# Kernel tuning notes

Hardware: AMD Instinct MI355X
Metric: run time of the kernel (lower is better)

The kernel has to match this reference:

```python
import jax, jax.numpy as jnp
import numpy as np

N, M, H, EMB, F = 2000, 32, 64, 32, 32   # nodes, neighbors, hidden, emb_dim, node_feat_dim
T, B, HOR = 12, 4, 12                     # seq_len, batch, horizon
K = 2                                     # tcn kernel
L_SAGE = 2
DILS = (1, 2)                             # dilations for the 2 TCN blocks


def _causal_conv(x, w, b, d):
    # x: (BN, C, T), w: (C_out, C_in, K) -- causal via left padding (K-1)*d
    y = jax.lax.conv_general_dilated(
        x, w, window_strides=(1,), padding=[((K - 1) * d, 0)],
        rhs_dilation=(d,), dimension_numbers=('NCH', 'OIH', 'NCH'))
    return y + b[None, :, None]


def setup_inputs() -> dict:
    key = jax.random.key(0)
    ks = jax.random.split(key, 32)
    s = 0.05
    def g(i, shape):
        return jax.random.normal(ks[i], shape, dtype=jnp.float32) * s
    return dict(
        inputs=jax.random.normal(ks[0], (T, B, N), dtype=jnp.float32),
        node_feas=jax.random.normal(ks[1], (N, F), dtype=jnp.float32),
        node_index=jax.random.randint(ks[2], (N, M), 0, N),
        # NodeEmbeddingMLP (fc3/fc4/fc5)
        w_fc3=g(3, (F, H)), b_fc3=jnp.zeros((H,), jnp.float32),
        w_fc4=g(4, (H, H)), b_fc4=jnp.zeros((H,), jnp.float32),
        w_fc5=g(5, (H, EMB)), b_fc5=jnp.zeros((EMB,), jnp.float32),
        # node_hidden_proj
        w_nhp=g(6, (EMB, H)), b_nhp=jnp.zeros((H,), jnp.float32),
        # attention (no bias)
        w_q=g(7, (EMB, H)), w_k=g(8, (EMB, H)),
        # input_proj
        w_in=g(9, (1, H)), b_in=jnp.zeros((H,), jnp.float32),
        # GraphSAGE layers (stacked)
        sage_w_self=g(10, (L_SAGE, H, H)), sage_b_self=jnp.zeros((L_SAGE, H), jnp.float32),
        sage_w_neigh=g(11, (L_SAGE, H, H)), sage_b_neigh=jnp.zeros((L_SAGE, H), jnp.float32),
        # TCN: 2 temporal blocks, each with conv1/conv2 (OIH layout)
        tcn_w1=g(12, (2, H, H, K)), tcn_b1=jnp.zeros((2, H), jnp.float32),
        tcn_w2=g(13, (2, H, H, K)), tcn_b2=jnp.zeros((2, H), jnp.float32),
        # scalar gate + output head
        w_gate=g(14, (H, 1)), b_gate=jnp.zeros((1,), jnp.float32),
        w_out=g(15, (H, HOR)), b_out=jnp.zeros((HOR,), jnp.float32),
    )


def reference(inputs, node_feas, node_index,
              w_fc3, b_fc3, w_fc4, b_fc4, w_fc5, b_fc5,
              w_nhp, b_nhp, w_q, w_k, w_in, b_in,
              sage_w_self, sage_b_self, sage_w_neigh, sage_b_neigh,
              tcn_w1, tcn_b1, tcn_w2, tcn_b2,
              w_gate, b_gate, w_out, b_out):
    # --- node embedding MLP ---
    e = jax.nn.relu(node_feas @ w_fc3 + b_fc3)
    e = jax.nn.relu(e @ w_fc4 + b_fc4)
    e = e @ w_fc5 + b_fc5                                  # (N, EMB)

    # --- attention over sampled neighbors (learned slim adjacency) ---
    q = e @ w_q                                            # (N, H)
    k = e[node_index] @ w_k                                # (N, M, H)
    scores = jnp.einsum('nh,nmh->nm', q, k) / jnp.sqrt(jnp.float32(H))
    w_adj = jax.nn.softmax(scores, axis=1)                 # (N, M) rows sum to 1

    node_hidden = e @ w_nhp + b_nhp                        # (N, H)

    # --- reshape inputs: (T, B, N) -> (B, T, N, 1) ---
    x = jnp.transpose(inputs, (1, 0, 2)).reshape(B, T, N, 1)
    x_proj = x @ w_in + b_in                               # (B, T, N, H)
    fused = x_proj + node_hidden                           # broadcast (N, H)
    h = fused.reshape(B * T, N, H)

    # --- GraphSAGE encoder: gather neighbors, weighted aggregate ---
    for l in range(L_SAGE):
        nb = h[:, node_index]                              # (B*T, N, M, H) irregular gather
        agg = jnp.einsum('nm,bnmh->bnh', w_adj, nb)        # (B*T, N, H)
        h = jax.nn.relu(h @ sage_w_self[l] + sage_b_self[l]
                        + agg @ sage_w_neigh[l] + sage_b_neigh[l])

    mid_output = h.reshape(B, T, N, H)

    # --- TCN over time per node: (B*N, H, T) ---
    ht = jnp.transpose(mid_output, (0, 2, 3, 1)).reshape(B * N, H, T)
    for l in range(2):
        res = ht
        y = jax.nn.relu(_causal_conv(ht, tcn_w1[l], tcn_b1[l], DILS[l]))
        y = jax.nn.relu(_causal_conv(y, tcn_w2[l], tcn_b2[l], DILS[l]))
        ht = jax.nn.relu(y + res)

    h_t = ht[:, :, -1]                                     # (B*N, H) last step temporal
    h_s = mid_output[:, -1].reshape(B * N, H)              # (B*N, H) last step spatial
    gate = jax.nn.sigmoid(h_t @ w_gate + b_gate)           # (B*N, 1) scalar gate
    fused_out = gate * h_t + (1.0 - gate) * h_s

    out = fused_out @ w_out + b_out                        # (B*N, HOR)
    outputs = out.reshape(B, N, HOR).transpose(2, 0, 1).reshape(HOR, B, N)
    return outputs, mid_output, w_adj
```

## Files before the change

kernel.cpp:

```cpp
#include <hip/hip_runtime.h>
#include <math.h>


__global__ __launch_bounds__(256) void k_embed(
    const float* __restrict__ nf, const float* __restrict__ inputs,
    const float* __restrict__ w3, const float* __restrict__ b3,
    const float* __restrict__ w4, const float* __restrict__ b4,
    const float* __restrict__ w5, const float* __restrict__ b5,
    const float* __restrict__ wq, const float* __restrict__ wk,
    const float* __restrict__ wn, const float* __restrict__ bn,
    const float* __restrict__ b_in,
    const float* __restrict__ tw1, const float* __restrict__ tw2,
    const float* __restrict__ sws, const float* __restrict__ swn,
    float2* __restrict__ wtx, float4* __restrict__ wsg,
    float* __restrict__ qo, float* __restrict__ eko, float* __restrict__ nho,
    float* __restrict__ xT)
{
    const int tid = threadIdx.x;
    if (tid < 192) {
        const int id = blockIdx.x * 192 + tid;
        const int t = id / 8000, rem = id % 8000;
        const int b = rem / 2000, n2 = rem % 2000;
        xT[n2 * 48 + b * 12 + t] = inputs[id];
    }
    if (blockIdx.x < 64) {
        const int id = blockIdx.x * 256 + tid;
        const int c = id >> 12, rr = id & 4095;
        const int i = rr >> 6, o = rr & 63;
        const float* src = (c == 0) ? tw1 : (c == 1) ? tw2
                         : (c == 2) ? tw1 + 8192 : tw2 + 8192;
        wtx[id] = make_float2(src[o * 128 + i * 2], src[o * 128 + i * 2 + 1]);
    } else if (blockIdx.x < 80) {
        const int id = (blockIdx.x - 64) * 256 + tid;
        const int l = id >> 11, rr = id & 2047;
        const int k2 = rr >> 6, h = rr & 63;
        const float* S = sws + l * 4096;
        const float* Nn = swn + l * 4096;
        wsg[id] = make_float4(S[(2 * k2) * 64 + h],     Nn[(2 * k2) * 64 + h],
                              S[(2 * k2 + 1) * 64 + h], Nn[(2 * k2 + 1) * 64 + h]);
    }
    const int lane = tid & 63;
    const int n = blockIdx.x * 4 + (tid >> 6);

    float nfv = 0.f;
    if (lane < 32) nfv = nf[n * 32 + lane];

    float e1 = b3[lane];
#pragma unroll
    for (int f = 0; f < 32; ++f)
        e1 = fmaf(__shfl(nfv, f), w3[f * 64 + lane], e1);
    e1 = fmaxf(e1, 0.f);

    float e2 = b4[lane];
#pragma unroll
    for (int f = 0; f < 64; ++f)
        e2 = fmaf(__shfl(e1, f), w4[f * 64 + lane], e2);
    e2 = fmaxf(e2, 0.f);

    const int c = lane & 31;
    float ev = b5[c];
#pragma unroll
    for (int f = 0; f < 64; ++f)
        ev = fmaf(__shfl(e2, f), w5[f * 32 + c], ev);

    float qv = 0.f, ekv = 0.f, nhv = bn[lane] + b_in[lane];
#pragma unroll
    for (int f = 0; f < 32; ++f) {
        float e = __shfl(ev, f);
        qv  = fmaf(e, wq[f * 64 + lane], qv);
        ekv = fmaf(e, wk[f * 64 + lane], ekv);
        nhv = fmaf(e, wn[f * 64 + lane], nhv);
    }
    qo [n * 64 + lane] = qv;
    eko[n * 64 + lane] = ekv;
    nho[n * 64 + lane] = nhv;
}

__global__ __launch_bounds__(256) void k_front(
    const float* __restrict__ q, const float* __restrict__ ek,
    const float* __restrict__ xT, const float* __restrict__ nh2,
    const int* __restrict__ nidx,
    const float* __restrict__ sws, const float* __restrict__ sbs,
    const float* __restrict__ swn, const float* __restrict__ sbn,
    const float* __restrict__ w_in, const float4* __restrict__ wsg,
    float* __restrict__ wadj, float2* __restrict__ xa,
    float* __restrict__ base1, float* __restrict__ vecs)
{
    const int tid = threadIdx.x;
    const int lane = tid & 63, wave = tid >> 6;
    if (blockIdx.x == 500) {
        if (wave == 0) {
            const float wv = w_in[lane];
            float s1 = 0.f, n1 = 0.f;
#pragma unroll
            for (int k = 0; k < 64; ++k) {
                const float wkk = __shfl(wv, k);
                s1 = fmaf(wkk, sws[k * 64 + lane], s1);
                n1 = fmaf(wkk, swn[k * 64 + lane], n1);
            }
            vecs[lane] = s1; vecs[64 + lane] = n1;
        }
        return;
    }
    __shared__ __align__(16) float2 pair[4][64];
    const int n = blockIdx.x * 4 + wave;

    int j = 0;
    if (lane < 32) j = nidx[n * 32 + lane];
    float w;
    {
        const float4* qr = (const float4*)(q + n * 64);
        const float4* er = (const float4*)(ek + j * 64);
        float s = 0.f;
#pragma unroll
        for (int u = 0; u < 16; ++u) {
            const float4 a = qr[u], b = er[u];
            s = fmaf(a.x, b.x, s); s = fmaf(a.y, b.y, s);
            s = fmaf(a.z, b.z, s); s = fmaf(a.w, b.w, s);
        }
        s *= 0.125f;
        float mx = s;
#pragma unroll
        for (int d = 16; d >= 1; d >>= 1) mx = fmaxf(mx, __shfl_xor(mx, d));
        const float ex = expf(s - mx);
        float sum = ex;
#pragma unroll
        for (int d = 16; d >= 1; d >>= 1) sum += __shfl_xor(sum, d);
        w = ex / sum;
        if (lane < 32) wadj[n * 32 + lane] = w;
    }
    float ax = 0.f, anh = 0.f;
    const bool act = lane < 48;
#pragma unroll 8
    for (int m = 0; m < 32; ++m) {
        const int jm = __shfl(j, m);
        const float wm = __shfl(w, m);
        const float xv = act ? xT[jm * 48 + lane] : 0.f;
        ax  = fmaf(wm, xv, ax);
        anh = fmaf(wm, nh2[jm * 64 + lane], anh);
    }
    if (act) xa[n * 48 + lane] = make_float2(xT[n * 48 + lane], ax);
    pair[wave][lane] = make_float2(nh2[n * 64 + lane], anh);
    __syncthreads();

    float acc = sbs[lane] + sbn[lane];
    const float2* pw = pair[wave];
#pragma unroll
    for (int k2 = 0; k2 < 32; ++k2) {
        const float4 wv = wsg[k2 * 64 + lane];
        const float4 sv = *(const float4*)(pw + k2 * 2);
        acc = fmaf(sv.x, wv.x, acc); acc = fmaf(sv.y, wv.y, acc);
        acc = fmaf(sv.z, wv.z, acc); acc = fmaf(sv.w, wv.w, acc);
    }
    base1[n * 64 + lane] = acc;
}

__global__ __launch_bounds__(512, 8) void k_sage2(
    const float* __restrict__ base1, const float2* __restrict__ xa,
    const float* __restrict__ vecs,
    const int* __restrict__ nidx, const float* __restrict__ wadj,
    const float4* __restrict__ wsg2,
    const float* __restrict__ sbs, const float* __restrict__ sbn,
    float* __restrict__ mid)
{
    __shared__ __align__(16) float2 svp[48][64];
    const int tid = threadIdx.x, lane = tid & 63;
    const int wave = __builtin_amdgcn_readfirstlane(tid >> 6);
    const int n = blockIdx.x;
    const int bt0 = wave * 6;

    const float s1 = vecs[lane], n1 = vecs[64 + lane];
    const float bs = base1[n * 64 + lane];

    float agg[6] = {0.f, 0.f, 0.f, 0.f, 0.f, 0.f};
#pragma unroll 8
    for (int m = 0; m < 32; ++m) {
        const int j = nidx[n * 32 + m];
        const float w = wadj[n * 32 + m];
        const float bj = base1[j * 64 + lane];
        const float4* xr = (const float4*)(xa + j * 48 + bt0);
        const float4 p0 = xr[0], p1 = xr[1], p2 = xr[2];
        float t;
        t = fmaf(p0.x, s1, fmaf(p0.y, n1, bj)); agg[0] = fmaf(w, fmaxf(t, 0.f), agg[0]);
        t = fmaf(p0.z, s1, fmaf(p0.w, n1, bj)); agg[1] = fmaf(w, fmaxf(t, 0.f), agg[1]);
        t = fmaf(p1.x, s1, fmaf(p1.y, n1, bj)); agg[2] = fmaf(w, fmaxf(t, 0.f), agg[2]);
        t = fmaf(p1.z, s1, fmaf(p1.w, n1, bj)); agg[3] = fmaf(w, fmaxf(t, 0.f), agg[3]);
        t = fmaf(p2.x, s1, fmaf(p2.y, n1, bj)); agg[4] = fmaf(w, fmaxf(t, 0.f), agg[4]);
        t = fmaf(p2.z, s1, fmaf(p2.w, n1, bj)); agg[5] = fmaf(w, fmaxf(t, 0.f), agg[5]);
    }
    {
        const float4* xs = (const float4*)(xa + n * 48 + bt0);
        const float4 q0 = xs[0], q1 = xs[1], q2 = xs[2];
        svp[bt0 + 0][lane] = make_float2(fmaxf(fmaf(q0.x, s1, fmaf(q0.y, n1, bs)), 0.f), agg[0]);
        svp[bt0 + 1][lane] = make_float2(fmaxf(fmaf(q0.z, s1, fmaf(q0.w, n1, bs)), 0.f), agg[1]);
        svp[bt0 + 2][lane] = make_float2(fmaxf(fmaf(q1.x, s1, fmaf(q1.y, n1, bs)), 0.f), agg[2]);
        svp[bt0 + 3][lane] = make_float2(fmaxf(fmaf(q1.z, s1, fmaf(q1.w, n1, bs)), 0.f), agg[3]);
        svp[bt0 + 4][lane] = make_float2(fmaxf(fmaf(q2.x, s1, fmaf(q2.y, n1, bs)), 0.f), agg[4]);
        svp[bt0 + 5][lane] = make_float2(fmaxf(fmaf(q2.z, s1, fmaf(q2.w, n1, bs)), 0.f), agg[5]);
    }
    const float b2 = sbs[64 + lane] + sbn[64 + lane];
    float acc[6] = {b2, b2, b2, b2, b2, b2};
    const float4* wp = wsg2 + lane;
    const float2* s0 = svp[bt0];
#pragma unroll
    for (int k2 = 0; k2 < 32; ++k2) {
        const float4 w4 = wp[k2 * 64];
        const float4 v0 = *(const float4*)(s0 + 0 * 64 + k2 * 2);
        const float4 v1 = *(const float4*)(s0 + 1 * 64 + k2 * 2);
        const float4 v2 = *(const float4*)(s0 + 2 * 64 + k2 * 2);
        const float4 v3 = *(const float4*)(s0 + 3 * 64 + k2 * 2);
        const float4 v4 = *(const float4*)(s0 + 4 * 64 + k2 * 2);
        const float4 v5 = *(const float4*)(s0 + 5 * 64 + k2 * 2);
        acc[0] = fmaf(v0.x, w4.x, fmaf(v0.y, w4.y, fmaf(v0.z, w4.z, fmaf(v0.w, w4.w, acc[0]))));
        acc[1] = fmaf(v1.x, w4.x, fmaf(v1.y, w4.y, fmaf(v1.z, w4.z, fmaf(v1.w, w4.w, acc[1]))));
        acc[2] = fmaf(v2.x, w4.x, fmaf(v2.y, w4.y, fmaf(v2.z, w4.z, fmaf(v2.w, w4.w, acc[2]))));
        acc[3] = fmaf(v3.x, w4.x, fmaf(v3.y, w4.y, fmaf(v3.z, w4.z, fmaf(v3.w, w4.w, acc[3]))));
        acc[4] = fmaf(v4.x, w4.x, fmaf(v4.y, w4.y, fmaf(v4.z, w4.z, fmaf(v4.w, w4.w, acc[4]))));
        acc[5] = fmaf(v5.x, w4.x, fmaf(v5.y, w4.y, fmaf(v5.z, w4.z, fmaf(v5.w, w4.w, acc[5]))));
    }
#pragma unroll
    for (int r = 0; r < 6; ++r)
        mid[((bt0 + r) * 2000 + n) * 64 + lane] = fmaxf(acc[r], 0.f);
}

__global__ __launch_bounds__(256, 4) void k_tcn(
    const float* __restrict__ mid, const float2* __restrict__ wt,
    const float* __restrict__ tb1, const float* __restrict__ tb2,
    const float* __restrict__ wgate, const float* __restrict__ bgate,
    const float* __restrict__ wout, const float* __restrict__ bout,
    float* __restrict__ outp)
{
    __shared__ __align__(16) float buf[4][2][7][68];
    const int tid = threadIdx.x, lane = tid & 63;
    const int wv = __builtin_amdgcn_readfirstlane(tid >> 6);
    const int sb = blockIdx.x * 8 + wv * 2;
    const int b = sb / 2000, n0 = sb - b * 2000;
    const float* __restrict__ xb = mid + ((long)(b * 12) * 2000 + n0) * 64;

    float r[2][3];
#pragma unroll
    for (int s = 0; s < 2; ++s) {
#pragma unroll
        for (int u = 0; u < 7; ++u) {
            const float v = xb[(5 + u) * 128000 + s * 64 + lane];
            buf[wv][s][u][lane] = v;
            if (u == 2) r[s][0] = v;
            if (u == 4) r[s][1] = v;
            if (u == 6) r[s][2] = v;
        }
    }
    __syncthreads();

    const float bs1 = tb1[lane];
    float y1[2][6];
#pragma unroll
    for (int s = 0; s < 2; ++s)
#pragma unroll
        for (int j = 0; j < 6; ++j) y1[s][j] = bs1;
#pragma unroll 4
    for (int ig = 0; ig < 16; ++ig) {
        float2 w0 = wt[(ig * 4 + 0) * 64 + lane];
        float2 w1 = wt[(ig * 4 + 1) * 64 + lane];
        float2 w2 = wt[(ig * 4 + 2) * 64 + lane];
        float2 w3 = wt[(ig * 4 + 3) * 64 + lane];
#pragma unroll
        for (int s = 0; s < 2; ++s) {
            float4 xu[7];
#pragma unroll
            for (int u = 0; u < 7; ++u)
                xu[u] = *(const float4*)&buf[wv][s][u][ig * 4];
#pragma unroll
            for (int j = 0; j < 6; ++j) {
                float acc = y1[s][j];
                acc = fmaf(w0.x, xu[j].x, acc); acc = fmaf(w0.y, xu[j + 1].x, acc);
                acc = fmaf(w1.x, xu[j].y, acc); acc = fmaf(w1.y, xu[j + 1].y, acc);
                acc = fmaf(w2.x, xu[j].z, acc); acc = fmaf(w2.y, xu[j + 1].z, acc);
                acc = fmaf(w3.x, xu[j].w, acc); acc = fmaf(w3.y, xu[j + 1].w, acc);
                y1[s][j] = acc;
            }
        }
    }
#pragma unroll
    for (int s = 0; s < 2; ++s)
#pragma unroll
        for (int j = 0; j < 6; ++j)
            buf[wv][s][j][lane] = fmaxf(y1[s][j], 0.f);
    __syncthreads();

    const float bs2 = tb2[lane];
    float a[2][3];
#pragma unroll
    for (int s = 0; s < 2; ++s) { a[s][0] = bs2; a[s][1] = bs2; a[s][2] = bs2; }
#pragma unroll 4
    for (int ig = 0; ig < 16; ++ig) {
        float2 w0 = wt[4096 + (ig * 4 + 0) * 64 + lane];
        float2 w1 = wt[4096 + (ig * 4 + 1) * 64 + lane];
        float2 w2 = wt[4096 + (ig * 4 + 2) * 64 + lane];
        float2 w3 = wt[4096 + (ig * 4 + 3) * 64 + lane];
#pragma unroll
        for (int s = 0; s < 2; ++s) {
            float4 yv[6];
#pragma unroll
            for (int j = 0; j < 6; ++j)
                yv[j] = *(const float4*)&buf[wv][s][j][ig * 4];
#pragma unroll
            for (int v = 0; v < 3; ++v) {
                float acc = a[s][v];
                acc = fmaf(w0.x, yv[2*v].x, acc); acc = fmaf(w0.y, yv[2*v+1].x, acc);
                acc = fmaf(w1.x, yv[2*v].y, acc); acc = fmaf(w1.y, yv[2*v+1].y, acc);
                acc = fmaf(w2.x, yv[2*v].z, acc); acc = fmaf(w2.y, yv[2*v+1].z, acc);
                acc = fmaf(w3.x, yv[2*v].w, acc); acc = fmaf(w3.y, yv[2*v+1].w, acc);
                a[s][v] = acc;
            }
        }
    }
    float x22[2];
#pragma unroll
    for (int s = 0; s < 2; ++s) {
        const float x20 = fmaxf(fmaxf(a[s][0], 0.f) + r[s][0], 0.f);
        const float x21 = fmaxf(fmaxf(a[s][1], 0.f) + r[s][1], 0.f);
        x22[s]          = fmaxf(fmaxf(a[s][2], 0.f) + r[s][2], 0.f);
        buf[wv][s][0][lane] = x20;
        buf[wv][s][1][lane] = x21;
        buf[wv][s][2][lane] = x22[s];
    }
    __syncthreads();

    const float bs3 = tb1[64 + lane];
    float d[2][2];
#pragma unroll
    for (int s = 0; s < 2; ++s) { d[s][0] = bs3; d[s][1] = bs3; }
#pragma unroll 4
    for (int ig = 0; ig < 16; ++ig) {
        float2 w0 = wt[8192 + (ig * 4 + 0) * 64 + lane];
        float2 w1 = wt[8192 + (ig * 4 + 1) * 64 + lane];
        float2 w2 = wt[8192 + (ig * 4 + 2) * 64 + lane];
        float2 w3 = wt[8192 + (ig * 4 + 3) * 64 + lane];
#pragma unroll
        for (int s = 0; s < 2; ++s) {
            float4 x0 = *(const float4*)&buf[wv][s][0][ig * 4];
            float4 x1 = *(const float4*)&buf[wv][s][1][ig * 4];
            float4 x2 = *(const float4*)&buf[wv][s][2][ig * 4];
            float acc0 = d[s][0], acc1 = d[s][1];
            acc0 = fmaf(w0.x, x0.x, acc0); acc0 = fmaf(w0.y, x1.x, acc0);
            acc0 = fmaf(w1.x, x0.y, acc0); acc0 = fmaf(w1.y, x1.y, acc0);
            acc0 = fmaf(w2.x, x0.z, acc0); acc0 = fmaf(w2.y, x1.z, acc0);
            acc0 = fmaf(w3.x, x0.w, acc0); acc0 = fmaf(w3.y, x1.w, acc0);
            acc1 = fmaf(w0.x, x1.x, acc1); acc1 = fmaf(w0.y, x2.x, acc1);
            acc1 = fmaf(w1.x, x1.y, acc1); acc1 = fmaf(w1.y, x2.y, acc1);
            acc1 = fmaf(w2.x, x1.z, acc1); acc1 = fmaf(w2.y, x2.z, acc1);
            acc1 = fmaf(w3.x, x1.w, acc1); acc1 = fmaf(w3.y, x2.w, acc1);
            d[s][0] = acc0; d[s][1] = acc1;
        }
    }
#pragma unroll
    for (int s = 0; s < 2; ++s) {
        buf[wv][s][4][lane] = fmaxf(d[s][0], 0.f);
        buf[wv][s][5][lane] = fmaxf(d[s][1], 0.f);
    }
    __syncthreads();

    const float bs4 = tb2[64 + lane];
    float f[2] = {bs4, bs4};
#pragma unroll 4
    for (int ig = 0; ig < 16; ++ig) {
        float2 w0 = wt[12288 + (ig * 4 + 0) * 64 + lane];
        float2 w1 = wt[12288 + (ig * 4 + 1) * 64 + lane];
        float2 w2 = wt[12288 + (ig * 4 + 2) * 64 + lane];
        float2 w3 = wt[12288 + (ig * 4 + 3) * 64 + lane];
#pragma unroll
        for (int s = 0; s < 2; ++s) {
            float4 g0 = *(const float4*)&buf[wv][s][4][ig * 4];
            float4 g1 = *(const float4*)&buf[wv][s][5][ig * 4];
            float acc = f[s];
            acc = fmaf(w0.x, g0.x, acc); acc = fmaf(w0.y, g1.x, acc);
            acc = fmaf(w1.x, g0.y, acc); acc = fmaf(w1.y, g1.y, acc);
            acc = fmaf(w2.x, g0.z, acc); acc = fmaf(w2.y, g1.z, acc);
            acc = fmaf(w3.x, g0.w, acc); acc = fmaf(w3.y, g1.w, acc);
            f[s] = acc;
        }
    }

    const float wg = wgate[lane];
#pragma unroll
    for (int s = 0; s < 2; ++s) {
        const float ht = fmaxf(fmaxf(f[s], 0.f) + x22[s], 0.f);
        float p = ht * wg;
#pragma unroll
        for (int dd = 1; dd < 64; dd <<= 1) p += __shfl_xor(p, dd);
        const float g = 1.f / (1.f + expf(-(p + bgate[0])));
        buf[wv][s][6][lane] = g * ht + (1.f - g) * r[s][2];
    }
    __syncthreads();
    if (lane < 24) {
        const int s = lane / 12, h = lane - s * 12;
        float acc = bout[h];
#pragma unroll 4
        for (int ig = 0; ig < 16; ++ig) {
            const float4 f4 = *(const float4*)&buf[wv][s][6][ig * 4];
            acc = fmaf(f4.x, wout[(ig * 4 + 0) * 12 + h], acc);
            acc = fmaf(f4.y, wout[(ig * 4 + 1) * 12 + h], acc);
            acc = fmaf(f4.z, wout[(ig * 4 + 2) * 12 + h], acc);
            acc = fmaf(f4.w, wout[(ig * 4 + 3) * 12 + h], acc);
        }
        outp[h * 8000 + sb + s] = acc;
    }
}

extern "C" void kernel_launch(void* const* d_in, const int* in_sizes, int n_in,
                              void* d_out, int out_size, void* d_ws, size_t ws_size,
                              hipStream_t stream) {
    const float* inputs     = (const float*)d_in[0];
    const float* node_feas  = (const float*)d_in[1];
    const int*   node_index = (const int*)  d_in[2];
    const float* w_fc3 = (const float*)d_in[3];
    const float* b_fc3 = (const float*)d_in[4];
    const float* w_fc4 = (const float*)d_in[5];
    const float* b_fc4 = (const float*)d_in[6];
    const float* w_fc5 = (const float*)d_in[7];
    const float* b_fc5 = (const float*)d_in[8];
    const float* w_nhp = (const float*)d_in[9];
    const float* b_nhp = (const float*)d_in[10];
    const float* w_q   = (const float*)d_in[11];
    const float* w_k   = (const float*)d_in[12];
    const float* w_in  = (const float*)d_in[13];
    const float* b_in  = (const float*)d_in[14];
    const float* sws   = (const float*)d_in[15];
    const float* sbs   = (const float*)d_in[16];
    const float* swn   = (const float*)d_in[17];
    const float* sbn   = (const float*)d_in[18];
    const float* tw1   = (const float*)d_in[19];
    const float* tb1   = (const float*)d_in[20];
    const float* tw2   = (const float*)d_in[21];
    const float* tb2   = (const float*)d_in[22];
    const float* wgate = (const float*)d_in[23];
    const float* bgate = (const float*)d_in[24];
    const float* wout  = (const float*)d_in[25];
    const float* bout  = (const float*)d_in[26];

    float* out  = (float*)d_out;
    float* mid  = out + 96000;
    float* wadj = mid + 6144000;

    float*  q     = (float*)d_ws;
    float*  ek    = q     + 128000;
    float*  nh2   = ek    + 128000;
    float*  base1 = nh2   + 128000;
    float*  xT    = base1 + 128000;
    float2* xa    = (float2*)(xT + 96000);
    float*  vecs  = xT + 96000 + 192000;
    float2* wt    = (float2*)(vecs + 128);
    float4* wsg   = (float4*)(vecs + 128 + 32768);

    k_embed<<<500, 256, 0, stream>>>(node_feas, inputs, w_fc3, b_fc3, w_fc4, b_fc4,
                                     w_fc5, b_fc5, w_q, w_k, w_nhp, b_nhp, b_in,
                                     tw1, tw2, sws, swn, wt, wsg,
                                     q, ek, nh2, xT);
    k_front<<<501, 256, 0, stream>>>(q, ek, xT, nh2, node_index,
                                     sws, sbs, swn, sbn, w_in, wsg,
                                     wadj, xa, base1, vecs);
    k_sage2<<<2000, 512, 0, stream>>>(base1, xa, vecs, node_index, wadj,
                                      wsg + 2048, sbs, sbn, mid);
    k_tcn<<<1000, 256, 0, stream>>>(mid, wt, tb1, tb2,
                                    wgate, bgate, wout, bout, out);
}
```

Measured before the change: 114.6 us.

## Process one sequence per wavefront in TCN, drop block barriers, use float4 weights

```diff
diff --git a/kernel.cpp b/kernel.cpp
--- a/kernel.cpp
+++ b/kernel.cpp
@@ -12,7 +12,7 @@
     const float* __restrict__ b_in,
     const float* __restrict__ tw1, const float* __restrict__ tw2,
     const float* __restrict__ sws, const float* __restrict__ swn,
-    float2* __restrict__ wtx, float4* __restrict__ wsg,
+    float4* __restrict__ wt4, float4* __restrict__ wsg,
     float* __restrict__ qo, float* __restrict__ eko, float* __restrict__ nho,
     float* __restrict__ xT)
 {
@@ -23,15 +23,15 @@
         const int b = rem / 2000, n2 = rem % 2000;
         xT[n2 * 48 + b * 12 + t] = inputs[id];
     }
-    if (blockIdx.x < 64) {
+    if (blockIdx.x < 32) {
         const int id = blockIdx.x * 256 + tid;
-        const int c = id >> 12, rr = id & 4095;
-        const int i = rr >> 6, o = rr & 63;
+        const int c = id >> 11, rr = id & 2047;
+        const int p = rr >> 6, o = rr & 63;
         const float* src = (c == 0) ? tw1 : (c == 1) ? tw2
                          : (c == 2) ? tw1 + 8192 : tw2 + 8192;
-        wtx[id] = make_float2(src[o * 128 + i * 2], src[o * 128 + i * 2 + 1]);
-    } else if (blockIdx.x < 80) {
-        const int id = (blockIdx.x - 64) * 256 + tid;
+        wt4[id] = *(const float4*)(src + o * 128 + p * 4);
+    } else if (blockIdx.x < 48) {
+        const int id = (blockIdx.x - 32) * 256 + tid;
         const int l = id >> 11, rr = id & 2047;
         const int k2 = rr >> 6, h = rr & 63;
         const float* S = sws + l * 4096;
@@ -223,187 +223,136 @@
         mid[((bt0 + r) * 2000 + n) * 64 + lane] = fmaxf(acc[r], 0.f);
 }
 
-__global__ __launch_bounds__(256, 4) void k_tcn(
-    const float* __restrict__ mid, const float2* __restrict__ wt,
+__global__ __launch_bounds__(256, 8) void k_tcn(
+    const float* __restrict__ mid, const float4* __restrict__ wt4,
     const float* __restrict__ tb1, const float* __restrict__ tb2,
     const float* __restrict__ wgate, const float* __restrict__ bgate,
     const float* __restrict__ wout, const float* __restrict__ bout,
     float* __restrict__ outp)
 {
-    __shared__ __align__(16) float buf[4][2][7][68];
+    __shared__ __align__(16) float buf[4][7][68];
     const int tid = threadIdx.x, lane = tid & 63;
     const int wv = __builtin_amdgcn_readfirstlane(tid >> 6);
-    const int sb = blockIdx.x * 8 + wv * 2;
-    const int b = sb / 2000, n0 = sb - b * 2000;
-    const float* __restrict__ xb = mid + ((long)(b * 12) * 2000 + n0) * 64;
-
-    float r[2][3];
-#pragma unroll
-    for (int s = 0; s < 2; ++s) {
-#pragma unroll
-        for (int u = 0; u < 7; ++u) {
-            const float v = xb[(5 + u) * 128000 + s * 64 + lane];
-            buf[wv][s][u][lane] = v;
-            if (u == 2) r[s][0] = v;
-            if (u == 4) r[s][1] = v;
-            if (u == 6) r[s][2] = v;
-        }
-    }
-    __syncthreads();
+    const int seq = blockIdx.x * 4 + wv;
+    const int b = seq / 2000, n = seq - b * 2000;
+    const float* __restrict__ xb = mid + ((long)(b * 12) * 2000 + n) * 64;
+
+    float r0, r1, r2;
+#pragma unroll
+    for (int u = 0; u < 7; ++u) {
+        const float v = xb[(5 + u) * 128000 + lane];
+        buf[wv][u][lane] = v;
+        if (u == 2) r0 = v;
+        if (u == 4) r1 = v;
+        if (u == 6) r2 = v;
+    }
 
     const float bs1 = tb1[lane];
-    float y1[2][6];
-#pragma unroll
-    for (int s = 0; s < 2; ++s)
-#pragma unroll
-        for (int j = 0; j < 6; ++j) y1[s][j] = bs1;
+    float y1[6] = {bs1, bs1, bs1, bs1, bs1, bs1};
 #pragma unroll 4
     for (int ig = 0; ig < 16; ++ig) {
-        float2 w0 = wt[(ig * 4 + 0) * 64 + lane];
-        float2 w1 = wt[(ig * 4 + 1) * 64 + lane];
-        float2 w2 = wt[(ig * 4 + 2) * 64 + lane];
-        float2 w3 = wt[(ig * 4 + 3) * 64 + lane];
-#pragma unroll
-        for (int s = 0; s < 2; ++s) {
-            float4 xu[7];
-#pragma unroll
-            for (int u = 0; u < 7; ++u)
-                xu[u] = *(const float4*)&buf[wv][s][u][ig * 4];
-#pragma unroll
-            for (int j = 0; j < 6; ++j) {
-                float acc = y1[s][j];
-                acc = fmaf(w0.x, xu[j].x, acc); acc = fmaf(w0.y, xu[j + 1].x, acc);
-                acc = fmaf(w1.x, xu[j].y, acc); acc = fmaf(w1.y, xu[j + 1].y, acc);
-                acc = fmaf(w2.x, xu[j].z, acc); acc = fmaf(w2.y, xu[j + 1].z, acc);
-                acc = fmaf(w3.x, xu[j].w, acc); acc = fmaf(w3.y, xu[j + 1].w, acc);
-                y1[s][j] = acc;
-            }
+        const float4 wA = wt4[(ig * 2 + 0) * 64 + lane];
+        const float4 wB = wt4[(ig * 2 + 1) * 64 + lane];
+        float4 xu[7];
+#pragma unroll
+        for (int u = 0; u < 7; ++u)
+            xu[u] = *(const float4*)&buf[wv][u][ig * 4];
+#pragma unroll
+        for (int j = 0; j < 6; ++j) {
+            float acc = y1[j];
+            acc = fmaf(wA.x, xu[j].x, acc); acc = fmaf(wA.y, xu[j + 1].x, acc);
+            acc = fmaf(wA.z, xu[j].y, acc); acc = fmaf(wA.w, xu[j + 1].y, acc);
+            acc = fmaf(wB.x, xu[j].z, acc); acc = fmaf(wB.y, xu[j + 1].z, acc);
+            acc = fmaf(wB.z, xu[j].w, acc); acc = fmaf(wB.w, xu[j + 1].w, acc);
+            y1[j] = acc;
         }
     }
 #pragma unroll
-    for (int s = 0; s < 2; ++s)
-#pragma unroll
-        for (int j = 0; j < 6; ++j)
-            buf[wv][s][j][lane] = fmaxf(y1[s][j], 0.f);
-    __syncthreads();
+    for (int j = 0; j < 6; ++j)
+        buf[wv][j][lane] = fmaxf(y1[j], 0.f);
 
     const float bs2 = tb2[lane];
-    float a[2][3];
-#pragma unroll
-    for (int s = 0; s < 2; ++s) { a[s][0] = bs2; a[s][1] = bs2; a[s][2] = bs2; }
+    float a0 = bs2, a1 = bs2, a2 = bs2;
 #pragma unroll 4
     for (int ig = 0; ig < 16; ++ig) {
-        float2 w0 = wt[4096 + (ig * 4 + 0) * 64 + lane];
-        float2 w1 = wt[4096 + (ig * 4 + 1) * 64 + lane];
-        float2 w2 = wt[4096 + (ig * 4 + 2) * 64 + lane];
-        float2 w3 = wt[4096 + (ig * 4 + 3) * 64 + lane];
-#pragma unroll
-        for (int s = 0; s < 2; ++s) {
-            float4 yv[6];
-#pragma unroll
-            for (int j = 0; j < 6; ++j)
-                yv[j] = *(const float4*)&buf[wv][s][j][ig * 4];
-#pragma unroll
-            for (int v = 0; v < 3; ++v) {
-                float acc = a[s][v];
-                acc = fmaf(w0.x, yv[2*v].x, acc); acc = fmaf(w0.y, yv[2*v+1].x, acc);
-                acc = fmaf(w1.x, yv[2*v].y, acc); acc = fmaf(w1.y, yv[2*v+1].y, acc);
-                acc = fmaf(w2.x, yv[2*v].z, acc); acc = fmaf(w2.y, yv[2*v+1].z, acc);
-                acc = fmaf(w3.x, yv[2*v].w, acc); acc = fmaf(w3.y, yv[2*v+1].w, acc);
-                a[s][v] = acc;
-            }
-        }
-    }
-    float x22[2];
-#pragma unroll
-    for (int s = 0; s < 2; ++s) {
-        const float x20 = fmaxf(fmaxf(a[s][0], 0.f) + r[s][0], 0.f);
-        const float x21 = fmaxf(fmaxf(a[s][1], 0.f) + r[s][1], 0.f);
-        x22[s]          = fmaxf(fmaxf(a[s][2], 0.f) + r[s][2], 0.f);
-        buf[wv][s][0][lane] = x20;
-        buf[wv][s][1][lane] = x21;
-        buf[wv][s][2][lane] = x22[s];
-    }
-    __syncthreads();
+        const float4 wA = wt4[2048 + (ig * 2 + 0) * 64 + lane];
+        const float4 wB = wt4[2048 + (ig * 2 + 1) * 64 + lane];
+        float4 yv[6];
+#pragma unroll
+        for (int j = 0; j < 6; ++j)
+            yv[j] = *(const float4*)&buf[wv][j][ig * 4];
+        a0 = fmaf(wA.x, yv[0].x, a0); a0 = fmaf(wA.y, yv[1].x, a0);
+        a0 = fmaf(wA.z, yv[0].y, a0); a0 = fmaf(wA.w, yv[1].y, a0);
+        a0 = fmaf(wB.x, yv[0].z, a0); a0 = fmaf(wB.y, yv[1].z, a0);
+        a0 = fmaf(wB.z, yv[0].w, a0); a0 = fmaf(wB.w, yv[1].w, a0);
+        a1 = fmaf(wA.x, yv[2].x, a1); a1 = fmaf(wA.y, yv[3].x, a1);
+        a1 = fmaf(wA.z, yv[2].y, a1); a1 = fmaf(wA.w, yv[3].y, a1);
+        a1 = fmaf(wB.x, yv[2].z, a1); a1 = fmaf(wB.y, yv[3].z, a1);
+        a1 = fmaf(wB.z, yv[2].w, a1); a1 = fmaf(wB.w, yv[3].w, a1);
+        a2 = fmaf(wA.x, yv[4].x, a2); a2 = fmaf(wA.y, yv[5].x, a2);
+        a2 = fmaf(wA.z, yv[4].y, a2); a2 = fmaf(wA.w, yv[5].y, a2);
+        a2 = fmaf(wB.x, yv[4].z, a2); a2 = fmaf(wB.y, yv[5].z, a2);
+        a2 = fmaf(wB.z, yv[4].w, a2); a2 = fmaf(wB.w, yv[5].w, a2);
+    }
+    const float x20 = fmaxf(fmaxf(a0, 0.f) + r0, 0.f);
+    const float x21 = fmaxf(fmaxf(a1, 0.f) + r1, 0.f);
+    const float x22 = fmaxf(fmaxf(a2, 0.f) + r2, 0.f);
+    buf[wv][0][lane] = x20;
+    buf[wv][1][lane] = x21;
+    buf[wv][2][lane] = x22;
 
     const float bs3 = tb1[64 + lane];
-    float d[2][2];
-#pragma unroll
-    for (int s = 0; s < 2; ++s) { d[s][0] = bs3; d[s][1] = bs3; }
+    float d0 = bs3, d1 = bs3;
 #pragma unroll 4
     for (int ig = 0; ig < 16; ++ig) {
-        float2 w0 = wt[8192 + (ig * 4 + 0) * 64 + lane];
-        float2 w1 = wt[8192 + (ig * 4 + 1) * 64 + lane];
-        float2 w2 = wt[8192 + (ig * 4 + 2) * 64 + lane];
-        float2 w3 = wt[8192 + (ig * 4 + 3) * 64 + lane];
-#pragma unroll
-        for (int s = 0; s < 2; ++s) {
-            float4 x0 = *(const float4*)&buf[wv][s][0][ig * 4];
-            float4 x1 = *(const float4*)&buf[wv][s][1][ig * 4];
-            float4 x2 = *(const float4*)&buf[wv][s][2][ig * 4];
-            float acc0 = d[s][0], acc1 = d[s][1];
-            acc0 = fmaf(w0.x, x0.x, acc0); acc0 = fmaf(w0.y, x1.x, acc0);
-            acc0 = fmaf(w1.x, x0.y, acc0); acc0 = fmaf(w1.y, x1.y, acc0);
-            acc0 = fmaf(w2.x, x0.z, acc0); acc0 = fmaf(w2.y, x1.z, acc0);
-            acc0 = fmaf(w3.x, x0.w, acc0); acc0 = fmaf(w3.y, x1.w, acc0);
-            acc1 = fmaf(w0.x, x1.x, acc1); acc1 = fmaf(w0.y, x2.x, acc1);
-            acc1 = fmaf(w1.x, x1.y, acc1); acc1 = fmaf(w1.y, x2.y, acc1);
-            acc1 = fmaf(w2.x, x1.z, acc1); acc1 = fmaf(w2.y, x2.z, acc1);
-            acc1 = fmaf(w3.x, x1.w, acc1); acc1 = fmaf(w3.y, x2.w, acc1);
-            d[s][0] = acc0; d[s][1] = acc1;
-        }
-    }
-#pragma unroll
-    for (int s = 0; s < 2; ++s) {
-        buf[wv][s][4][lane] = fmaxf(d[s][0], 0.f);
-        buf[wv][s][5][lane] = fmaxf(d[s][1], 0.f);
-    }
-    __syncthreads();
+        const float4 wA = wt4[4096 + (ig * 2 + 0) * 64 + lane];
+        const float4 wB = wt4[4096 + (ig * 2 + 1) * 64 + lane];
+        const float4 x0 = *(const float4*)&buf[wv][0][ig * 4];
+        const float4 x1 = *(const float4*)&buf[wv][1][ig * 4];
+        const float4 x2 = *(const float4*)&buf[wv][2][ig * 4];
+        d0 = fmaf(wA.x, x0.x, d0); d0 = fmaf(wA.y, x1.x, d0);
+        d0 = fmaf(wA.z, x0.y, d0); d0 = fmaf(wA.w, x1.y, d0);
+        d0 = fmaf(wB.x, x0.z, d0); d0 = fmaf(wB.y, x1.z, d0);
+        d0 = fmaf(wB.z, x0.w, d0); d0 = fmaf(wB.w, x1.w, d0);
+        d1 = fmaf(wA.x, x1.x, d1); d1 = fmaf(wA.y, x2.x, d1);
+        d1 = fmaf(wA.z, x1.y, d1); d1 = fmaf(wA.w, x2.y, d1);
+        d1 = fmaf(wB.x, x1.z, d1); d1 = fmaf(wB.y, x2.z, d1);
+        d1 = fmaf(wB.z, x1.w, d1); d1 = fmaf(wB.w, x2.w, d1);
+    }
+    buf[wv][4][lane] = fmaxf(d0, 0.f);
+    buf[wv][5][lane] = fmaxf(d1, 0.f);
 
     const float bs4 = tb2[64 + lane];
-    float f[2] = {bs4, bs4};
+    float f = bs4;
 #pragma unroll 4
     for (int ig = 0; ig < 16; ++ig) {
-        float2 w0 = wt[12288 + (ig * 4 + 0) * 64 + lane];
-        float2 w1 = wt[12288 + (ig * 4 + 1) * 64 + lane];
-        float2 w2 = wt[12288 + (ig * 4 + 2) * 64 + lane];
-        float2 w3 = wt[12288 + (ig * 4 + 3) * 64 + lane];
-#pragma unroll
-        for (int s = 0; s < 2; ++s) {
-            float4 g0 = *(const float4*)&buf[wv][s][4][ig * 4];
-            float4 g1 = *(const float4*)&buf[wv][s][5][ig * 4];
-            float acc = f[s];
-            acc = fmaf(w0.x, g0.x, acc); acc = fmaf(w0.y, g1.x, acc);
-            acc = fmaf(w1.x, g0.y, acc); acc = fmaf(w1.y, g1.y, acc);
-            acc = fmaf(w2.x, g0.z, acc); acc = fmaf(w2.y, g1.z, acc);
-            acc = fmaf(w3.x, g0.w, acc); acc = fmaf(w3.y, g1.w, acc);
-            f[s] = acc;
-        }
-    }
-
-    const float wg = wgate[lane];
-#pragma unroll
-    for (int s = 0; s < 2; ++s) {
-        const float ht = fmaxf(fmaxf(f[s], 0.f) + x22[s], 0.f);
-        float p = ht * wg;
-#pragma unroll
-        for (int dd = 1; dd < 64; dd <<= 1) p += __shfl_xor(p, dd);
-        const float g = 1.f / (1.f + expf(-(p + bgate[0])));
-        buf[wv][s][6][lane] = g * ht + (1.f - g) * r[s][2];
-    }
-    __syncthreads();
-    if (lane < 24) {
-        const int s = lane / 12, h = lane - s * 12;
-        float acc = bout[h];
+        const float4 wA = wt4[6144 + (ig * 2 + 0) * 64 + lane];
+        const float4 wB = wt4[6144 + (ig * 2 + 1) * 64 + lane];
+        const float4 g0 = *(const float4*)&buf[wv][4][ig * 4];
+        const float4 g1 = *(const float4*)&buf[wv][5][ig * 4];
+        f = fmaf(wA.x, g0.x, f); f = fmaf(wA.y, g1.x, f);
+        f = fmaf(wA.z, g0.y, f); f = fmaf(wA.w, g1.y, f);
+        f = fmaf(wB.x, g0.z, f); f = fmaf(wB.y, g1.z, f);
+        f = fmaf(wB.z, g0.w, f); f = fmaf(wB.w, g1.w, f);
+    }
+
+    const float ht = fmaxf(fmaxf(f, 0.f) + x22, 0.f);
+    float p = ht * wgate[lane];
+#pragma unroll
+    for (int dd = 1; dd < 64; dd <<= 1) p += __shfl_xor(p, dd);
+    const float g = 1.f / (1.f + expf(-(p + bgate[0])));
+    buf[wv][6][lane] = g * ht + (1.f - g) * r2;
+    if (lane < 12) {
+        float acc = bout[lane];
 #pragma unroll 4
         for (int ig = 0; ig < 16; ++ig) {
-            const float4 f4 = *(const float4*)&buf[wv][s][6][ig * 4];
-            acc = fmaf(f4.x, wout[(ig * 4 + 0) * 12 + h], acc);
-            acc = fmaf(f4.y, wout[(ig * 4 + 1) * 12 + h], acc);
-            acc = fmaf(f4.z, wout[(ig * 4 + 2) * 12 + h], acc);
-            acc = fmaf(f4.w, wout[(ig * 4 + 3) * 12 + h], acc);
+            const float4 f4 = *(const float4*)&buf[wv][6][ig * 4];
+            acc = fmaf(f4.x, wout[(ig * 4 + 0) * 12 + lane], acc);
+            acc = fmaf(f4.y, wout[(ig * 4 + 1) * 12 + lane], acc);
+            acc = fmaf(f4.z, wout[(ig * 4 + 2) * 12 + lane], acc);
+            acc = fmaf(f4.w, wout[(ig * 4 + 3) * 12 + lane], acc);
         }
-        outp[h * 8000 + sb + s] = acc;
+        outp[lane * 8000 + seq] = acc;
     }
 }
 
@@ -449,18 +398,18 @@
     float*  xT    = base1 + 128000;
     float2* xa    = (float2*)(xT + 96000);
     float*  vecs  = xT + 96000 + 192000;
-    float2* wt    = (float2*)(vecs + 128);
+    float4* wt4   = (float4*)(vecs + 128);
     float4* wsg   = (float4*)(vecs + 128 + 32768);
 
     k_embed<<<500, 256, 0, stream>>>(node_feas, inputs, w_fc3, b_fc3, w_fc4, b_fc4,
                                      w_fc5, b_fc5, w_q, w_k, w_nhp, b_nhp, b_in,
-                                     tw1, tw2, sws, swn, wt, wsg,
+                                     tw1, tw2, sws, swn, wt4, wsg,
                                      q, ek, nh2, xT);
     k_front<<<501, 256, 0, stream>>>(q, ek, xT, nh2, node_index,
                                      sws, sbs, swn, sbn, w_in, wsg,
                                      wadj, xa, base1, vecs);
     k_sage2<<<2000, 512, 0, stream>>>(base1, xa, vecs, node_index, wadj,
                                       wsg + 2048, sbs, sbn, mid);
-    k_tcn<<<1000, 256, 0, stream>>>(mid, wt, tb1, tb2,
+    k_tcn<<<2000, 256, 0, stream>>>(mid, wt4, tb1, tb2,
                                     wgate, bgate, wout, bout, out);
 }
```

Result: no change. 116.3 us (+1.4%).
